# Performance work log

Hardware: AMD Instinct MI355X
Metric: run time of the kernel (lower is better)

Reference implementation:

```python
import jax, jax.numpy as jnp
import numpy as np

G = 16          # GroupNorm groups
EPS = 1e-5


def setup_inputs() -> dict:
    key = jax.random.key(0)
    ks = jax.random.split(key, 6)
    B, C, H, W = 2, 256, 96, 96
    O = 256
    x = jax.random.normal(ks[0], (B, C, H, W), dtype=jnp.float32)
    offset = jax.random.normal(ks[1], (B, 18, H, W), dtype=jnp.float32)
    mask = jax.random.uniform(ks[2], (B, 9, H, W), dtype=jnp.float32)
    fan_in = C * 9
    weight = jax.random.normal(ks[3], (O, C, 3, 3), dtype=jnp.float32) / np.sqrt(fan_in)
    bias = jnp.zeros((O,), dtype=jnp.float32)
    gamma = jnp.ones((O,), dtype=jnp.float32)
    beta = jnp.zeros((O,), dtype=jnp.float32)
    return {"x": x, "offset": offset, "mask": mask, "weight": weight,
            "bias": bias, "gamma": gamma, "beta": beta}


def _mdcn_gn(x, offset, mask, weight, bias, gamma, beta):
    B, C, H, W = x.shape
    O = weight.shape[0]
    K = 9
    # offsets: mmcv layout [y0,x0,y1,x1,...] per kernel point k = kh*3+kw
    off = offset.reshape(B, K, 2, H, W)
    off_y, off_x = off[:, :, 0], off[:, :, 1]            # [B,K,H,W]
    ky = (jnp.arange(K) // 3 - 1).astype(x.dtype)        # kernel dy, pad=1
    kx = (jnp.arange(K) % 3 - 1).astype(x.dtype)
    hh = jnp.arange(H, dtype=x.dtype)[:, None]
    ww = jnp.arange(W, dtype=x.dtype)[None, :]
    py = hh[None, None] + ky[:, None, None] + off_y      # [B,K,H,W] sample y
    px = ww[None, None] + kx[:, None, None] + off_x      # [B,K,H,W] sample x

    y0 = jnp.floor(py)
    x0 = jnp.floor(px)
    dy = py - y0
    dx = px - x0
    y0i = y0.astype(jnp.int32)
    x0i = x0.astype(jnp.int32)

    xf = x.reshape(B, C, H * W)

    def gather(yi, xi):
        # zero-padded bilinear corner: out-of-range corners contribute 0
        valid = ((yi >= 0) & (yi < H) & (xi >= 0) & (xi < W)).astype(x.dtype)
        yc = jnp.clip(yi, 0, H - 1)
        xc = jnp.clip(xi, 0, W - 1)
        idx = (yc * W + xc).reshape(B, 1, K * H * W)
        v = jnp.take_along_axis(xf, idx, axis=2).reshape(B, C, K, H, W)
        return v * valid.reshape(B, 1, K, H, W)

    w00 = ((1 - dy) * (1 - dx))[:, None]                 # [B,1,K,H,W]
    w01 = ((1 - dy) * dx)[:, None]
    w10 = (dy * (1 - dx))[:, None]
    w11 = (dy * dx)[:, None]
    val = (gather(y0i, x0i) * w00 + gather(y0i, x0i + 1) * w01 +
           gather(y0i + 1, x0i) * w10 + gather(y0i + 1, x0i + 1) * w11)
    val = val * mask[:, None]                            # modulation [B,C,K,H,W]

    out = jnp.einsum('ock,bckhw->bohw', weight.reshape(O, C, K), val)
    out = out + bias[None, :, None, None]

    # GroupNorm(16, O)
    xg = out.reshape(B, G, O // G, H, W)
    mean = xg.mean(axis=(2, 3, 4), keepdims=True)
    var = jnp.mean((xg - mean) ** 2, axis=(2, 3, 4), keepdims=True)
    xn = ((xg - mean) * jax.lax.rsqrt(var + EPS)).reshape(B, O, H, W)
    return xn * gamma[None, :, None, None] + beta[None, :, None, None]


def reference(x, offset, mask, weight, bias, gamma, beta):
    return _mdcn_gn(x, offset, mask, weight, bias, gamma, beta)
```

## Files before the change

### kernel.cpp

```cpp
#include <hip/hip_runtime.h>
#include <hip/hip_fp16.h>

typedef _Float16 f16;
typedef __attribute__((ext_vector_type(2))) _Float16 h2v;
typedef __attribute__((ext_vector_type(8))) _Float16 f16x8;
typedef __attribute__((ext_vector_type(4))) float f32x4;

#define HW_    9216
#define PADP   8
#define XP_    112
#define XPXP_  12544
#define NSTEP  72
#define NMT    288
#define XT_BYTES   12845056
#define BMAT_BYTES 1179648
#define ATILE_B    294912
#define A32_B      147456
#define OUTH_BYTES 9437184
#define PART_BYTES 24576

union U4 { uint4 u; h2v h[4]; f16x8 v; f16 f[8]; };
union U1 { unsigned u; h2v h; };
union UO { ushort4 s; f16 f[4]; };

__global__ __launch_bounds__(256) void k_zero(uint4* __restrict__ p) {
    int i = blockIdx.x*1024 + threadIdx.x;
    uint4 z = {0u,0u,0u,0u};
    p[i] = z; p[i+256] = z; p[i+512] = z; p[i+768] = z;
}

__global__ __launch_bounds__(256) void k_prep_x(const float* __restrict__ x, f16* __restrict__ xT) {
    __shared__ float tile[64 * 97];
    int blk = blockIdx.x;
    int cg  = blk & 3;
    int y   = (blk >> 2) % 96;
    int b   = blk / 384;
    int t   = threadIdx.x;
    const float* src = x + (((size_t)(b*256 + cg*64))*96 + y)*96;
    for (int e = t; e < 6144; e += 256) {
        int c = e / 96, wcol = e - c*96;
        tile[c*97 + wcol] = src[(size_t)c*HW_ + wcol];
    }
    __syncthreads();
    f16* dst = xT + ((size_t)b*XPXP_ + (size_t)(y+PADP)*XP_ + PADP)*256 + cg*64;
    for (int e = t; e < 6144; e += 256) {
        int wcol = e >> 6, c = e & 63;
        dst[(size_t)wcol*256 + c] = (f16)tile[c*97 + wcol];
    }
}

__global__ __launch_bounds__(256) void k_prep_w(const float* __restrict__ wgt, f16* __restrict__ bmat) {
    int id = blockIdx.x*256 + threadIdx.x;
    int o = id / 2304;
    int rem = id - o*2304;
    int c = rem / 9;
    int k = rem - c*9;
    int s  = k*8 + (c >> 5);
    int nw = o >> 6, fn = (o >> 4) & 3, r = o & 15;
    int kq = (c >> 3) & 3, e = c & 7;
    bmat[(size_t)s*8192 + nw*2048 + fn*512 + (kq*16 + r)*8 + e] = (f16)wgt[id];
}

__global__ __launch_bounds__(256, 6) void k_sample(
        const f16* __restrict__ xT, const float* __restrict__ offs,
        const float* __restrict__ maskp, f16* __restrict__ Ag, int mt0, int nblk)
{
    __shared__ int   geo_i[64];
    __shared__ uint4 geo_w[64];

    int blk0 = blockIdx.x;
    int blk  = (blk0 & 7)*(nblk >> 3) + (blk0 >> 3);
    int mtl  = blk / 9;
    int k    = blk - mtl*9;
    int mt   = mt0 + mtl;
    int b    = mt / 144;

    int tid = threadIdx.x;
    if (tid < 64) {
        int hw = mt*64 + tid - b*HW_;
        int h = hw / 96, w = hw - h*96;
        float offy = offs[((size_t)b*18 + 2*k    )*HW_ + hw];
        float offx = offs[((size_t)b*18 + 2*k + 1)*HW_ + hw];
        float mv   = maskp[((size_t)b*9 + k)*HW_ + hw];
        int ky = k/3 - 1, kx = k - (k/3)*3 - 1;
        float py = (float)(h + ky) + offy;
        float px = (float)(w + kx) + offx;
        py = fminf(fmaxf(py, -7.5f), 102.4f);
        px = fminf(fmaxf(px, -7.5f), 102.4f);
        float y0 = floorf(py), x0 = floorf(px);
        float dy = py - y0,   dx = px - x0;
        geo_i[tid] = (((int)y0 + PADP)*XP_ + ((int)x0 + PADP)) << 9;
        float w00v = (1.f-dy)*(1.f-dx)*mv, w01v = (1.f-dy)*dx*mv;
        float w10v = dy*(1.f-dx)*mv,       w11v = dy*dx*mv;
        U1 p0, p1, p2, p3;
        p0.h = h2v{(f16)w00v, (f16)w00v};
        p1.h = h2v{(f16)w01v, (f16)w01v};
        p2.h = h2v{(f16)w10v, (f16)w10v};
        p3.h = h2v{(f16)w11v, (f16)w11v};
        geo_w[tid] = uint4{p0.u, p1.u, p2.u, p3.u};
    }
    __syncthreads();

    const char* xbC = (const char*)xT + (size_t)b*XPXP_*512;
    char* dst = (char*)Ag + (size_t)mtl*ATILE_B;

    #pragma unroll
    for (int j = 0; j < 8; ++j) {
        int item = tid + j*256;
        int row = item >> 5, chunk = item & 31;
        const char* p = xbC + geo_i[row] + (chunk << 4);
        U4 t0, t1, t2, t3, oo;
        t0.u = *(const uint4*)(p);
        t1.u = *(const uint4*)(p + 512);
        t2.u = *(const uint4*)(p + XP_*512);
        t3.u = *(const uint4*)(p + XP_*512 + 512);
        U4 w4; w4.u = geo_w[row];
        h2v w00 = w4.h[0], w01 = w4.h[1], w10 = w4.h[2], w11 = w4.h[3];
        #pragma unroll
        for (int q = 0; q < 4; ++q)
            oo.h[q] = w00*t0.h[q] + w01*t1.h[q] + w10*t2.h[q] + w11*t3.h[q];
        int s = k*8 + (chunk >> 2);
        size_t off = (size_t)(row >> 5)*A32_B + (size_t)s*2048
                   + ((row >> 4) & 1)*1024 + (((chunk & 3)*16 + (row & 15)) << 4);
        *(uint4*)(dst + off) = oo.u;
    }
}

#define MFMA16(a,b,c) __builtin_amdgcn_mfma_f32_16x16x32_f16(a,b,c,0,0,0)

#define DECLSET(P) uint4 A##P##0,A##P##1,A##P##2,A##P##3,A##P##4,A##P##5, \
                         B##P##0,B##P##1,B##P##2,B##P##3

#define LOADSET(P, s_) do { \
    const char* pa_ = aB + (size_t)(s_)*2048; \
    const char* pb_ = bB + (size_t)(s_)*16384; \
    A##P##0 = *(const uint4*)(pa_); \
    A##P##1 = *(const uint4*)(pa_ + 1024); \
    A##P##2 = *(const uint4*)(pa_ + A32_B); \
    A##P##3 = *(const uint4*)(pa_ + A32_B + 1024); \
    A##P##4 = *(const uint4*)(pa_ + 2*A32_B); \
    A##P##5 = *(const uint4*)(pa_ + 2*A32_B + 1024); \
    B##P##0 = *(const uint4*)(pb_); \
    B##P##1 = *(const uint4*)(pb_ + 1024); \
    B##P##2 = *(const uint4*)(pb_ + 2048); \
    B##P##3 = *(const uint4*)(pb_ + 3072); \
  } while (0)

#define MMROW(P, jm, Areg) do { \
    U4 xa_, xb_; xa_.u = Areg; \
    xb_.u = B##P##0; acc[jm][0] = MFMA16(xa_.v, xb_.v, acc[jm][0]); \
    xb_.u = B##P##1; acc[jm][1] = MFMA16(xa_.v, xb_.v, acc[jm][1]); \
    xb_.u = B##P##2; acc[jm][2] = MFMA16(xa_.v, xb_.v, acc[jm][2]); \
    xb_.u = B##P##3; acc[jm][3] = MFMA16(xa_.v, xb_.v, acc[jm][3]); \
  } while (0)

#define MMSET(P) do { \
    MMROW(P, 0, A##P##0); MMROW(P, 1, A##P##1); MMROW(P, 2, A##P##2); \
    MMROW(P, 3, A##P##3); MMROW(P, 4, A##P##4); MMROW(P, 5, A##P##5); \
  } while (0)

__global__ __launch_bounds__(64, 1) void k_gemm(
        const f16* __restrict__ Ag, const f16* __restrict__ bmat,
        const float* __restrict__ bias, f16* __restrict__ outh,
        float* __restrict__ part, int row0, int nwv)
{
    int w0 = blockIdx.x;
    int w  = (w0 & 7)*(nwv >> 3) + (w0 >> 3);
    int mwl = w >> 2, nw = w & 3;
    int lane = threadIdx.x;

    const char* aB = (const char*)Ag + (size_t)mwl*(3*A32_B) + lane*16;
    const char* bB = (const char*)bmat + nw*4096 + lane*16;

    f32x4 acc[6][4];
    #pragma unroll
    for (int i = 0; i < 6; ++i)
        #pragma unroll
        for (int j = 0; j < 4; ++j) acc[i][j] = (f32x4){0.f,0.f,0.f,0.f};

    DECLSET(0); DECLSET(1); DECLSET(2);

    LOADSET(0, 0);
    LOADSET(1, 1);
    LOADSET(2, 2);

    for (int s = 0; s < 69; s += 3) {
        MMSET(0);  LOADSET(0, s+3);
        MMSET(1);  LOADSET(1, s+4);
        MMSET(2);  LOADSET(2, s+5);
    }
    MMSET(0);
    MMSET(1);
    MMSET(2);

    int grow = row0 + mwl*96;
    int mwg  = grow / 96;
    int b    = grow / HW_;
    int hwb  = grow - b*HW_;
    int ol   = lane & 15;
    int qr   = (lane >> 4) << 2;
    #pragma unroll
    for (int jm = 0; jm < 6; ++jm) {
        #pragma unroll
        for (int fn = 0; fn < 4; ++fn) {
            int o = nw*64 + fn*16 + ol;
            float bv = bias[o];
            f32x4 a = acc[jm][fn];
            a[0] += bv; a[1] += bv; a[2] += bv; a[3] += bv;
            acc[jm][fn] = a;
            UO ov;
            ov.f[0] = (f16)a[0]; ov.f[1] = (f16)a[1];
            ov.f[2] = (f16)a[2]; ov.f[3] = (f16)a[3];
            *(ushort4*)(outh + ((size_t)(b*256 + o))*HW_ + hwb + jm*16 + qr) = ov.s;
        }
    }
    #pragma unroll
    for (int fn = 0; fn < 4; ++fn) {
        float s1 = 0.f, s2 = 0.f;
        #pragma unroll
        for (int jm = 0; jm < 6; ++jm) {
            f32x4 a = acc[jm][fn];
            s1 += a[0]+a[1]+a[2]+a[3];
            s2 += a[0]*a[0]+a[1]*a[1]+a[2]*a[2]+a[3]*a[3];
        }
        #pragma unroll
        for (int m = 32; m > 0; m >>= 1) {
            s1 += __shfl_xor(s1, m);
            s2 += __shfl_xor(s2, m);
        }
        if (lane == 0) {
            part[((size_t)mwg*16 + nw*4 + fn)*2]     = s1;
            part[((size_t)mwg*16 + nw*4 + fn)*2 + 1] = s2;
        }
    }
}

__global__ __launch_bounds__(256) void k_finalize(const float* __restrict__ part, float* __restrict__ stats) {
    int bg = blockIdx.x, b = bg >> 4, g = bg & 15;
    float s1 = 0.f, s2 = 0.f;
    if (threadIdx.x < 96) {
        const float* p = part + ((size_t)(b*96 + threadIdx.x)*16 + g)*2;
        s1 = p[0]; s2 = p[1];
    }
    __shared__ float a1[256], a2[256];
    a1[threadIdx.x] = s1; a2[threadIdx.x] = s2;
    __syncthreads();
    for (int off = 128; off > 0; off >>= 1) {
        if (threadIdx.x < off) { a1[threadIdx.x] += a1[threadIdx.x+off]; a2[threadIdx.x] += a2[threadIdx.x+off]; }
        __syncthreads();
    }
    if (threadIdx.x == 0) {
        float inv_n = 1.f/147456.f;
        float mean = a1[0]*inv_n;
        float var  = fmaxf(a2[0]*inv_n - mean*mean, 0.f);
        stats[bg*2]   = mean;
        stats[bg*2+1] = rsqrtf(var + 1e-5f);
    }
}

__global__ __launch_bounds__(256) void k_norm(const f16* __restrict__ outh, float* __restrict__ out,
                                              const float* __restrict__ stats,
                                              const float* __restrict__ gamma, const float* __restrict__ beta) {
    int i8 = blockIdx.x*256 + threadIdx.x;
    int p  = i8 / 1152;
    int o  = p & 255;
    float mean = stats[(p>>4)*2], rstd = stats[(p>>4)*2 + 1];
    float ga = gamma[o]*rstd, be = beta[o] - mean*rstd*gamma[o];
    U4 v; v.u = ((const uint4*)outh)[i8];
    float4 o0, o1;
    o0.x = (float)v.f[0]*ga + be; o0.y = (float)v.f[1]*ga + be;
    o0.z = (float)v.f[2]*ga + be; o0.w = (float)v.f[3]*ga + be;
    o1.x = (float)v.f[4]*ga + be; o1.y = (float)v.f[5]*ga + be;
    o1.z = (float)v.f[6]*ga + be; o1.w = (float)v.f[7]*ga + be;
    ((float4*)out)[i8*2]     = o0;
    ((float4*)out)[i8*2 + 1] = o1;
}

extern "C" void kernel_launch(void* const* d_in, const int* in_sizes, int n_in,
                              void* d_out, int out_size, void* d_ws, size_t ws_size,
                              hipStream_t stream) {
    const float* x      = (const float*)d_in[0];
    const float* offset = (const float*)d_in[1];
    const float* mask   = (const float*)d_in[2];
    const float* weight = (const float*)d_in[3];
    const float* bias   = (const float*)d_in[4];
    const float* gamma  = (const float*)d_in[5];
    const float* beta   = (const float*)d_in[6];
    float* out = (float*)d_out;

    char* ws = (char*)d_ws;
    f16*   xT    = (f16*)ws;
    f16*   bmat  = (f16*)(ws + XT_BYTES);
    float* part  = (float*)(ws + XT_BYTES + BMAT_BYTES);
    float* stats = (float*)(ws + XT_BYTES + BMAT_BYTES + PART_BYTES);
    f16*   outh  = (f16*)(ws + XT_BYTES + BMAT_BYTES + PART_BYTES + 256);
    char*  Ag    = ws + XT_BYTES + BMAT_BYTES + PART_BYTES + 256 + OUTH_BYTES;

    size_t needA = (size_t)NMT * ATILE_B;
    size_t base  = (size_t)XT_BYTES + BMAT_BYTES + PART_BYTES + 256 + OUTH_BYTES;
    size_t avail = ws_size > base ? ws_size - base : 0;
    int P = (avail >= needA) ? 1 : ((avail >= needA/2) ? 2 : 4);

    k_zero<<<784, 256, 0, stream>>>((uint4*)xT);
    k_prep_x<<<768, 256, 0, stream>>>(x, xT);
    k_prep_w<<<2304, 256, 0, stream>>>(weight, bmat);
    int mtn = NMT / P;
    int nwv = 768 / P;
    for (int p = 0; p < P; ++p) {
        k_sample<<<mtn*9, 256, 0, stream>>>(xT, offset, mask, (f16*)Ag, p*mtn, mtn*9);
        k_gemm<<<nwv, 64, 0, stream>>>((f16*)Ag, bmat, bias, outh, part, p*mtn*64, nwv);
    }
    k_finalize<<<32, 256, 0, stream>>>(part, stats);
    k_norm<<<2304, 256, 0, stream>>>(outh, out, stats, gamma, beta);
}
```

Baseline: 87.48 us.

## Restructure GEMM into 4-wave blocks with 64-row tiles per wave

The GEMM changes from single-wave 64-thread blocks, each computing a 96x64 output tile, to 256-thread blocks of four waves, each wave computing a 64x64 tile. All four waves share the same weight column tile. The smaller per-wave tile lowers accumulator and register pressure and allows more waves per CU, at the cost of less reuse of the weight fragments per FLOP. The GroupNorm partial-sum buffer and the finalize reduction are resized to match the new 64-row granularity (144 partials per batch).

```diff
diff --git a/kernel.cpp b/kernel.cpp
--- a/kernel.cpp
+++ b/kernel.cpp
@@ -17,7 +17,7 @@
 #define ATILE_B    294912
 #define A32_B      147456
 #define OUTH_BYTES 9437184
-#define PART_BYTES 24576
+#define PART_BYTES 36864
 
 union U4 { uint4 u; h2v h[4]; f16x8 v; f16 f[8]; };
 union U1 { unsigned u; h2v h; };
@@ -128,7 +128,7 @@
 
 #define MFMA16(a,b,c) __builtin_amdgcn_mfma_f32_16x16x32_f16(a,b,c,0,0,0)
 
-#define DECLSET(P) uint4 A##P##0,A##P##1,A##P##2,A##P##3,A##P##4,A##P##5, \
+#define DECLSET(P) uint4 A##P##0,A##P##1,A##P##2,A##P##3, \
                          B##P##0,B##P##1,B##P##2,B##P##3
 
 #define LOADSET(P, s_) do { \
@@ -138,8 +138,6 @@
     A##P##1 = *(const uint4*)(pa_ + 1024); \
     A##P##2 = *(const uint4*)(pa_ + A32_B); \
     A##P##3 = *(const uint4*)(pa_ + A32_B + 1024); \
-    A##P##4 = *(const uint4*)(pa_ + 2*A32_B); \
-    A##P##5 = *(const uint4*)(pa_ + 2*A32_B + 1024); \
     B##P##0 = *(const uint4*)(pb_); \
     B##P##1 = *(const uint4*)(pb_ + 1024); \
     B##P##2 = *(const uint4*)(pb_ + 2048); \
@@ -155,26 +153,27 @@
   } while (0)
 
 #define MMSET(P) do { \
-    MMROW(P, 0, A##P##0); MMROW(P, 1, A##P##1); MMROW(P, 2, A##P##2); \
-    MMROW(P, 3, A##P##3); MMROW(P, 4, A##P##4); MMROW(P, 5, A##P##5); \
+    MMROW(P, 0, A##P##0); MMROW(P, 1, A##P##1); \
+    MMROW(P, 2, A##P##2); MMROW(P, 3, A##P##3); \
   } while (0)
 
-__global__ __launch_bounds__(64, 1) void k_gemm(
+__global__ __launch_bounds__(256, 2) void k_gemm(
         const f16* __restrict__ Ag, const f16* __restrict__ bmat,
         const float* __restrict__ bias, f16* __restrict__ outh,
-        float* __restrict__ part, int row0, int nwv)
+        float* __restrict__ part, int row0, int nblk)
 {
-    int w0 = blockIdx.x;
-    int w  = (w0 & 7)*(nwv >> 3) + (w0 >> 3);
-    int mwl = w >> 2, nw = w & 3;
-    int lane = threadIdx.x;
-
-    const char* aB = (const char*)Ag + (size_t)mwl*(3*A32_B) + lane*16;
-    const char* bB = (const char*)bmat + nw*4096 + lane*16;
-
-    f32x4 acc[6][4];
+    int b0 = blockIdx.x;
+    int bb = (b0 & 7)*(nblk >> 3) + (b0 >> 3);
+    int mt = bb >> 2, nt = bb & 3;
+    int lane = threadIdx.x & 63;
+    int wid  = threadIdx.x >> 6;
+
+    const char* aB = (const char*)Ag + (size_t)(mt*4 + wid)*ATILE_B + lane*16;
+    const char* bB = (const char*)bmat + nt*4096 + lane*16;
+
+    f32x4 acc[4][4];
     #pragma unroll
-    for (int i = 0; i < 6; ++i)
+    for (int i = 0; i < 4; ++i)
         #pragma unroll
         for (int j = 0; j < 4; ++j) acc[i][j] = (f32x4){0.f,0.f,0.f,0.f};
 
@@ -193,17 +192,17 @@
     MMSET(1);
     MMSET(2);
 
-    int grow = row0 + mwl*96;
-    int mwg  = grow / 96;
+    int grow = row0 + (mt*4 + wid)*64;
+    int t64  = grow >> 6;
     int b    = grow / HW_;
     int hwb  = grow - b*HW_;
     int ol   = lane & 15;
     int qr   = (lane >> 4) << 2;
     #pragma unroll
-    for (int jm = 0; jm < 6; ++jm) {
+    for (int jm = 0; jm < 4; ++jm) {
         #pragma unroll
         for (int fn = 0; fn < 4; ++fn) {
-            int o = nw*64 + fn*16 + ol;
+            int o = nt*64 + fn*16 + ol;
             float bv = bias[o];
             f32x4 a = acc[jm][fn];
             a[0] += bv; a[1] += bv; a[2] += bv; a[3] += bv;
@@ -218,7 +217,7 @@
     for (int fn = 0; fn < 4; ++fn) {
         float s1 = 0.f, s2 = 0.f;
         #pragma unroll
-        for (int jm = 0; jm < 6; ++jm) {
+        for (int jm = 0; jm < 4; ++jm) {
             f32x4 a = acc[jm][fn];
             s1 += a[0]+a[1]+a[2]+a[3];
             s2 += a[0]*a[0]+a[1]*a[1]+a[2]*a[2]+a[3]*a[3];
@@ -229,8 +228,8 @@
             s2 += __shfl_xor(s2, m);
         }
         if (lane == 0) {
-            part[((size_t)mwg*16 + nw*4 + fn)*2]     = s1;
-            part[((size_t)mwg*16 + nw*4 + fn)*2 + 1] = s2;
+            part[((size_t)t64*16 + nt*4 + fn)*2]     = s1;
+            part[((size_t)t64*16 + nt*4 + fn)*2 + 1] = s2;
         }
     }
 }
@@ -238,8 +237,8 @@
 __global__ __launch_bounds__(256) void k_finalize(const float* __restrict__ part, float* __restrict__ stats) {
     int bg = blockIdx.x, b = bg >> 4, g = bg & 15;
     float s1 = 0.f, s2 = 0.f;
-    if (threadIdx.x < 96) {
-        const float* p = part + ((size_t)(b*96 + threadIdx.x)*16 + g)*2;
+    if (threadIdx.x < 144) {
+        const float* p = part + ((size_t)(b*144 + threadIdx.x)*16 + g)*2;
         s1 = p[0]; s2 = p[1];
     }
     __shared__ float a1[256], a2[256];
@@ -305,10 +304,9 @@
     k_prep_x<<<768, 256, 0, stream>>>(x, xT);
     k_prep_w<<<2304, 256, 0, stream>>>(weight, bmat);
     int mtn = NMT / P;
-    int nwv = 768 / P;
     for (int p = 0; p < P; ++p) {
         k_sample<<<mtn*9, 256, 0, stream>>>(xT, offset, mask, (f16*)Ag, p*mtn, mtn*9);
-        k_gemm<<<nwv, 64, 0, stream>>>((f16*)Ag, bmat, bias, outh, part, p*mtn*64, nwv);
+        k_gemm<<<mtn, 256, 0, stream>>>((f16*)Ag, bmat, bias, outh, part, p*mtn*64, mtn);
     }
     k_finalize<<<32, 256, 0, stream>>>(part, stats);
     k_norm<<<2304, 256, 0, stream>>>(outh, out, stats, gamma, beta);
```

Result: slower. 102.6 us (+17.2%).
